# Kernel tuning notes

Hardware: AMD Instinct MI355X
Metric: run time of the kernel (lower is better)

The kernel has to match this reference:

```python
import jax, jax.numpy as jnp
import numpy as np

CLIP_FRAMES = 16
CLIP_STRIDE = 8
D_CODE = 256
K_CODE = 8192
ENC_DIM = 128 * CLIP_FRAMES * 4 * 4  # 32768
EPS = 1e-5


def setup_inputs() -> dict:
    key = jax.random.key(0)
    ks = jax.random.split(key, 16)
    rn = lambda k, s, sc: (jax.random.normal(k, s, jnp.float32) * sc)
    inp = {}
    inp['x'] = jax.random.normal(ks[0], (4, 3, 64, 96, 96), jnp.float32)
    inp['conv1_w'] = rn(ks[1], (32, 3, 3, 3, 3), 0.1)
    inp['conv1_b'] = jnp.zeros((32,), jnp.float32)
    inp['bn1_g'] = jnp.ones((32,), jnp.float32)
    inp['bn1_b'] = jnp.zeros((32,), jnp.float32)
    inp['conv2_w'] = rn(ks[2], (64, 32, 3, 3, 3), 0.05)
    inp['conv2_b'] = jnp.zeros((64,), jnp.float32)
    inp['bn2_g'] = jnp.ones((64,), jnp.float32)
    inp['bn2_b'] = jnp.zeros((64,), jnp.float32)
    inp['conv3_w'] = rn(ks[3], (128, 64, 3, 3, 3), 0.04)
    inp['conv3_b'] = jnp.zeros((128,), jnp.float32)
    inp['bn3_g'] = jnp.ones((128,), jnp.float32)
    inp['bn3_b'] = jnp.zeros((128,), jnp.float32)
    inp['proj_w'] = rn(ks[4], (D_CODE, ENC_DIM), 0.005)
    inp['proj_b'] = jnp.zeros((D_CODE,), jnp.float32)
    inp['codebook'] = jax.random.uniform(ks[5], (K_CODE, D_CODE), jnp.float32, -1.0 / K_CODE, 1.0 / K_CODE)
    inp['gru_w_ih'] = rn(ks[6], (3 * D_CODE, D_CODE), 0.05)
    inp['gru_w_hh'] = rn(ks[7], (3 * D_CODE, D_CODE), 0.05)
    inp['gru_b_ih'] = jnp.zeros((3 * D_CODE,), jnp.float32)
    inp['gru_b_hh'] = jnp.zeros((3 * D_CODE,), jnp.float32)
    return inp


def _conv3d(x, w, b):
    y = jax.lax.conv_general_dilated(x, w, (1, 1, 1), ((1, 1), (1, 1), (1, 1)),
                                     dimension_numbers=('NCDHW', 'OIDHW', 'NCDHW'))
    return y + b[None, :, None, None, None]


def _bn(x, g, b):
    # training-mode BatchNorm3d: batch stats over (N,D,H,W), biased variance
    m = x.mean(axis=(0, 2, 3, 4), keepdims=True)
    v = ((x - m) ** 2).mean(axis=(0, 2, 3, 4), keepdims=True)
    return g[None, :, None, None, None] * (x - m) * jax.lax.rsqrt(v + EPS) + b[None, :, None, None, None]


def _maxpool(x):
    return jax.lax.reduce_window(x, -jnp.inf, jax.lax.max, (1, 1, 1, 2, 2), (1, 1, 1, 2, 2), 'VALID')


def _adaptive_avgpool(x):
    # [N,128,16,24,24] -> [N,128,16,4,4]; 24/4=6 exact window
    s = jax.lax.reduce_window(x, 0.0, jax.lax.add, (1, 1, 1, 6, 6), (1, 1, 1, 6, 6), 'VALID')
    return s / 36.0


def _gru(xs, w_ih, w_hh, b_ih, b_hh):
    # torch GRU, batch_first, h0=0. xs: [B,L,D]
    B, L, D = xs.shape
    gx = jnp.einsum('bld,gd->blg', xs, w_ih) + b_ih  # [B,L,3D]

    def step(h, gx_t):
        gh = h @ w_hh.T + b_hh
        xr, xz, xn = jnp.split(gx_t, 3, axis=-1)
        hr, hz, hn = jnp.split(gh, 3, axis=-1)
        r = jax.nn.sigmoid(xr + hr)
        z = jax.nn.sigmoid(xz + hz)
        n = jnp.tanh(xn + r * hn)
        h2 = (1.0 - z) * n + z * h
        return h2, h2

    h0 = jnp.zeros((B, D), xs.dtype)
    _, ys = jax.lax.scan(step, h0, jnp.swapaxes(gx, 0, 1))
    return jnp.swapaxes(ys, 0, 1)  # [B,L,D]


def _forward(x, conv1_w, conv1_b, bn1_g, bn1_b, conv2_w, conv2_b, bn2_g, bn2_b,
             conv3_w, conv3_b, bn3_g, bn3_b, proj_w, proj_b, codebook,
             gru_w_ih, gru_w_hh, gru_b_ih, gru_b_hh):
    B, C, T, H, W = x.shape
    num_clips = max(1, (T - CLIP_FRAMES) // CLIP_STRIDE + 1)
    clips = jnp.stack([x[:, :, i * CLIP_STRIDE:i * CLIP_STRIDE + CLIP_FRAMES] for i in range(num_clips)])

    def encode(clip):  # clip: [B,3,16,96,96]; BN stats per-clip like the torch loop
        h = jax.nn.relu(_bn(_conv3d(clip, conv1_w, conv1_b), bn1_g, bn1_b))
        h = _maxpool(h)
        h = jax.nn.relu(_bn(_conv3d(h, conv2_w, conv2_b), bn2_g, bn2_b))
        h = _maxpool(h)
        h = jax.nn.relu(_bn(_conv3d(h, conv3_w, conv3_b), bn3_g, bn3_b))
        h = _adaptive_avgpool(h)            # [B,128,16,4,4]
        h = h.reshape(B, -1)                # [B, 32768]
        return h @ proj_w.T + proj_b        # [B, D_CODE]

    features = jnp.swapaxes(jax.vmap(encode)(clips), 0, 1)  # [B,L,D]
    L, D = features.shape[1], features.shape[2]

    # quantize: squared-Euclidean argmin (same argmin as torch.cdist p=2)
    flat = features.reshape(-1, D)
    d2 = (flat * flat).sum(-1, keepdims=True) - 2.0 * flat @ codebook.T + (codebook * codebook).sum(-1)
    token_indices = jnp.argmin(d2, axis=-1)
    quantized = codebook[token_indices].reshape(B, L, D)

    sg = jax.lax.stop_gradient
    commitment_loss = jnp.mean((features - sg(quantized)) ** 2)
    codebook_loss = jnp.mean((quantized - sg(features)) ** 2)
    context_features = _gru(quantized[:, :-1], gru_w_ih, gru_w_hh, gru_b_ih, gru_b_hh)
    context_loss = jnp.mean((context_features - features[:, 1:]) ** 2)
    vq_loss = commitment_loss + 0.25 * codebook_loss + 0.1 * context_loss
    return token_indices.reshape(B, L), quantized, commitment_loss, codebook_loss, context_loss, vq_loss


def reference(x, conv1_w, conv1_b, bn1_g, bn1_b, conv2_w, conv2_b, bn2_g, bn2_b,
              conv3_w, conv3_b, bn3_g, bn3_b, proj_w, proj_b, codebook,
              gru_w_ih, gru_w_hh, gru_b_ih, gru_b_hh):
    return _forward(x, conv1_w, conv1_b, bn1_g, bn1_b, conv2_w, conv2_b, bn2_g, bn2_b,
                    conv3_w, conv3_b, bn3_g, bn3_b, proj_w, proj_b, codebook,
                    gru_w_ih, gru_w_hh, gru_b_ih, gru_b_hh)
```

## Files before the change

### kernel.cpp

```cpp
#include <hip/hip_runtime.h>
#include <math.h>


typedef __attribute__((ext_vector_type(8))) short short8;
typedef __attribute__((ext_vector_type(4))) float f32x4;

__device__ inline unsigned short f2bf(float x) {
    unsigned int u = __float_as_uint(x);
    u += 0x7FFFu + ((u >> 16) & 1u);
    return (unsigned short)(u >> 16);
}
__device__ inline float bf2f(unsigned short h) {
    return __uint_as_float(((unsigned int)h) << 16);
}
__device__ inline f32x4 vmax4(f32x4 a, f32x4 b) {
    return (f32x4){fmaxf(a.x, b.x), fmaxf(a.y, b.y), fmaxf(a.z, b.z), fmaxf(a.w, b.w)};
}
__device__ inline f32x4 vmin4(f32x4 a, f32x4 b) {
    return (f32x4){fminf(a.x, b.x), fminf(a.y, b.y), fminf(a.z, b.z), fminf(a.w, b.w)};
}

#define MF(d, a, b) d = __builtin_amdgcn_mfma_f32_16x16x32_bf16(a, b, d, 0, 0, 0)

#define C1LOADR(J) \
    f32x4 u = *(const f32x4*)(ip + (J) * 36); \
    f32x4 w4 = *(const f32x4*)(ip + (J) * 36 + 4); \
    f32x4 sA = u; \
    f32x4 sB = __builtin_shufflevector(u, w4, 1, 2, 3, 4); \
    f32x4 sC = __builtin_shufflevector(u, w4, 2, 3, 4, 5);
#define C1UPD0(I) a0_##I += wa0 * sA + wa1 * sB + wa2 * sC; a1_##I += wb0 * sA + wb1 * sB + wb2 * sC;
#define C1UPD1(I) a0_##I += wa3 * sA + wa4 * sB + wa5 * sC; a1_##I += wb3 * sA + wb4 * sB + wb5 * sC;
#define C1UPD2(I) a0_##I += wa6 * sA + wa7 * sB + wa8 * sC; a1_##I += wb6 * sA + wb7 * sB + wb8 * sC;

__launch_bounds__(256, 3)
__global__ void conv1k(const float* __restrict__ x, const float* __restrict__ wgt,
                       const float* __restrict__ bias, float* __restrict__ pmax,
                       float* __restrict__ pmin, float* __restrict__ stats, int t0) {
    int bb = blockIdx.x;
    int xt = bb % 3; int yt = (bb / 3) % 4; int t = (bb / 12) % 16; int n = bb / 192;
    int x0 = xt * 32, y0 = yt * 24;
    __shared__ float tile[9 * 936];
    __shared__ float wl[3456];
    __shared__ float sst[64];
    int tid = threadIdx.x;
    for (int i = tid; i < 3456; i += 256) {
        int idx = i % 12; int r = i / 12;
        int co = r & 31; int p = r >> 5;
        wl[i] = idx < 9 ? wgt[co * 81 + p * 9 + idx] : 0.f;
    }
    if (tid < 64) sst[tid] = 0.f;
    for (int i = tid; i < 7956; i += 256) {
        int p = i / 884; int rem = i % 884;
        int r = rem / 34, cl = rem % 34;
        int ci = p / 3, kt = p % 3;
        int lt = t + kt - 1;
        int yy = y0 + r - 1, xx = x0 + cl - 1;
        float v = 0.f;
        if (lt >= 0 && lt <= 15 && yy >= 0 && yy < 96 && xx >= 0 && xx < 96)
            v = x[((size_t)(n * 3 + ci) * 64 + (t0 + lt)) * 9216 + yy * 96 + cl + x0 - 1];
        tile[p * 936 + r * 36 + cl] = v;
    }
    __syncthreads();

    int cg = tid & 15;
    int co0 = cg * 2;
    float bv0 = bias[co0], bv1 = bias[co0 + 1];
    float ls0 = 0.f, lq0 = 0.f, ls1 = 0.f, lq1 = 0.f;
    size_t nt48 = (size_t)(n * 16 + t) * 48;

    #pragma unroll 1
    for (int rr = 0; rr < 3; ++rr) {
        int sp = rr * 16 + (tid >> 4);
        int tx = sp & 7, ty = sp >> 3;
        f32x4 a0_0 = (f32x4)bv0, a0_1 = (f32x4)bv0, a0_2 = (f32x4)bv0, a0_3 = (f32x4)bv0;
        f32x4 a1_0 = (f32x4)bv1, a1_1 = (f32x4)bv1, a1_2 = (f32x4)bv1, a1_3 = (f32x4)bv1;

        #pragma unroll 1
        for (int p = 0; p < 9; ++p) {
            const float* wpk = wl + ((p * 32 + co0) * 12);
            f32x4 wv0 = *(const f32x4*)(wpk);
            f32x4 wv1 = *(const f32x4*)(wpk + 4);
            f32x4 wv2 = *(const f32x4*)(wpk + 8);
            f32x4 wv3 = *(const f32x4*)(wpk + 12);
            f32x4 wv4 = *(const f32x4*)(wpk + 16);
            f32x4 wv5 = *(const f32x4*)(wpk + 20);
            float wa0 = wv0.x, wa1 = wv0.y, wa2 = wv0.z, wa3 = wv0.w;
            float wa4 = wv1.x, wa5 = wv1.y, wa6 = wv1.z, wa7 = wv1.w;
            float wa8 = wv2.x;
            float wb0 = wv3.x, wb1 = wv3.y, wb2 = wv3.z, wb3 = wv3.w;
            float wb4 = wv4.x, wb5 = wv4.y, wb6 = wv4.z, wb7 = wv4.w;
            float wb8 = wv5.x;
            const float* ip = tile + p * 936 + (ty * 4) * 36 + tx * 4;
            { C1LOADR(0) C1UPD0(0) }
            { C1LOADR(1) C1UPD0(1) C1UPD1(0) }
            { C1LOADR(2) C1UPD0(2) C1UPD1(1) C1UPD2(0) }
            { C1LOADR(3) C1UPD0(3) C1UPD1(2) C1UPD2(1) }
            { C1LOADR(4) C1UPD1(3) C1UPD2(2) }
            { C1LOADR(5) C1UPD2(3) }
        }

        f32x4 s4 = a0_0 + a0_1 + a0_2 + a0_3;
        ls0 += s4.x + s4.y + s4.z + s4.w;
        f32x4 q4 = a0_0 * a0_0 + a0_1 * a0_1 + a0_2 * a0_2 + a0_3 * a0_3;
        lq0 += q4.x + q4.y + q4.z + q4.w;
        f32x4 s5 = a1_0 + a1_1 + a1_2 + a1_3;
        ls1 += s5.x + s5.y + s5.z + s5.w;
        f32x4 q5 = a1_0 * a1_0 + a1_1 * a1_1 + a1_2 * a1_2 + a1_3 * a1_3;
        lq1 += q5.x + q5.y + q5.z + q5.w;

        f32x4 mx0a = vmax4(a0_0, a0_1), mx0b = vmax4(a0_2, a0_3);
        f32x4 mn0a = vmin4(a0_0, a0_1), mn0b = vmin4(a0_2, a0_3);
        f32x4 mx1a = vmax4(a1_0, a1_1), mx1b = vmax4(a1_2, a1_3);
        f32x4 mn1a = vmin4(a1_0, a1_1), mn1b = vmin4(a1_2, a1_3);
        size_t row0 = (nt48 + (size_t)(yt * 12 + ty * 2)) * 1536 + (size_t)(xt * 16 + tx * 2) * 32 + co0;
        size_t row1 = row0 + 1536;
        *(float2*)(pmax + row0)      = make_float2(fmaxf(mx0a.x, mx0a.y), fmaxf(mx1a.x, mx1a.y));
        *(float2*)(pmax + row0 + 32) = make_float2(fmaxf(mx0a.z, mx0a.w), fmaxf(mx1a.z, mx1a.w));
        *(float2*)(pmax + row1)      = make_float2(fmaxf(mx0b.x, mx0b.y), fmaxf(mx1b.x, mx1b.y));
        *(float2*)(pmax + row1 + 32) = make_float2(fmaxf(mx0b.z, mx0b.w), fmaxf(mx1b.z, mx1b.w));
        *(float2*)(pmin + row0)      = make_float2(fminf(mn0a.x, mn0a.y), fminf(mn1a.x, mn1a.y));
        *(float2*)(pmin + row0 + 32) = make_float2(fminf(mn0a.z, mn0a.w), fminf(mn1a.z, mn1a.w));
        *(float2*)(pmin + row1)      = make_float2(fminf(mn0b.x, mn0b.y), fminf(mn1b.x, mn1b.y));
        *(float2*)(pmin + row1 + 32) = make_float2(fminf(mn0b.z, mn0b.w), fminf(mn1b.z, mn1b.w));
    }

    ls0 += __shfl_xor(ls0, 16, 64); ls0 += __shfl_xor(ls0, 32, 64);
    lq0 += __shfl_xor(lq0, 16, 64); lq0 += __shfl_xor(lq0, 32, 64);
    ls1 += __shfl_xor(ls1, 16, 64); ls1 += __shfl_xor(ls1, 32, 64);
    lq1 += __shfl_xor(lq1, 16, 64); lq1 += __shfl_xor(lq1, 32, 64);
    if ((tid & 63) < 16) {
        atomicAdd(&sst[co0 * 2], ls0);
        atomicAdd(&sst[co0 * 2 + 1], lq0);
        atomicAdd(&sst[co0 * 2 + 2], ls1);
        atomicAdd(&sst[co0 * 2 + 3], lq1);
    }
    __syncthreads();
    if (tid < 64) atomicAdd(&stats[tid], sst[tid]);
}

__global__ void bnpool1b(const float* __restrict__ pmax, const float* __restrict__ pmin,
                         const float* __restrict__ st, const float* __restrict__ gam,
                         const float* __restrict__ bet,
                         unsigned short* __restrict__ phi, unsigned short* __restrict__ plo) {
    int i = blockIdx.x * 256 + threadIdx.x;
    int c8 = i & 3; int xo = (i >> 2) % 48; int yo = (i / 192) % 48;
    int t = (i / 9216) % 16; int n = i / 147456;
    size_t base = (((size_t)(n * 16 + t) * 48 + yo) * 48 + xo) * 32 + c8 * 8;
    union { unsigned short s[8]; uint4 v; } Uh, Ul;
    #pragma unroll
    for (int j = 0; j < 8; ++j) {
        int ch = c8 * 8 + j;
        float mean = st[ch * 2] * (1.f / 589824.f);
        float var  = st[ch * 2 + 1] * (1.f / 589824.f) - mean * mean;
        var = var < 0.f ? 0.f : var;
        float sc = gam[ch] / sqrtf(var + 1e-5f);
        float sh = bet[ch] - mean * sc;
        float pv = sc >= 0.f ? pmax[base + j] : pmin[base + j];
        float v = fmaxf(sc * pv + sh, 0.f);
        Uh.s[j] = f2bf(v);
        Ul.s[j] = f2bf(v - bf2f(Uh.s[j]));
    }
    size_t off = ((((size_t)n * 18 + t + 1) * 50 + yo + 1) * 52 + (xo + 1)) * 32 + c8 * 8;
    *(uint4*)(phi + off) = Uh.v;
    *(uint4*)(plo + off) = Ul.v;
}

#define DECLW(S) short8 S##a0, S##a1, S##a2, S##a3, S##l0, S##l1, S##l2, S##l3;

#define LOADW2(S, KY, KX) { \
    const unsigned short* wb_ = wkt + ((KY) * 3 + (KX)) * 4096; \
    S##a0 = *(const short8*)(wb_);        S##a1 = *(const short8*)(wb_ + 512); \
    S##a2 = *(const short8*)(wb_ + 1024); S##a3 = *(const short8*)(wb_ + 1536); \
    S##l0 = *(const short8*)(wb_ + 2048); S##l1 = *(const short8*)(wb_ + 2560); \
    S##l2 = *(const short8*)(wb_ + 3072); S##l3 = *(const short8*)(wb_ + 3584); \
}

#define COMPUTE2(S, KY, KX) { \
    int row_ = wv + (KY); \
    int xx0_ = (KX) + c, xx1_ = 16 + (KX) + c, xx2_ = 32 + (KX) + c; \
    int sq0_ = (q ^ (xx0_ & 3) ^ ((xx0_ >> 2) & 3)) << 3; \
    int sq1_ = (q ^ (xx1_ & 3) ^ ((xx1_ >> 2) & 3)) << 3; \
    int sq2_ = (q ^ (xx2_ & 3) ^ ((xx2_ >> 2) & 3)) << 3; \
    short8 bh0_ = *(const short8*)(tin + ((row_ * 52 + xx0_) << 5) + sq0_); \
    short8 bl0_ = *(const short8*)(tin + (((6 + row_) * 52 + xx0_) << 5) + sq0_); \
    short8 bh1_ = *(const short8*)(tin + ((row_ * 52 + xx1_) << 5) + sq1_); \
    short8 bl1_ = *(const short8*)(tin + (((6 + row_) * 52 + xx1_) << 5) + sq1_); \
    short8 bh2_ = *(const short8*)(tin + ((row_ * 52 + xx2_) << 5) + sq2_); \
    short8 bl2_ = *(const short8*)(tin + (((6 + row_) * 52 + xx2_) << 5) + sq2_); \
    MF(acc[0][0], S##a0, bh0_); MF(acc[0][0], S##a0, bl0_); MF(acc[0][0], S##l0, bh0_); \
    MF(acc[0][1], S##a0, bh1_); MF(acc[0][1], S##a0, bl1_); MF(acc[0][1], S##l0, bh1_); \
    MF(acc[0][2], S##a0, bh2_); MF(acc[0][2], S##a0, bl2_); MF(acc[0][2], S##l0, bh2_); \
    MF(acc[1][0], S##a1, bh0_); MF(acc[1][0], S##a1, bl0_); MF(acc[1][0], S##l1, bh0_); \
    MF(acc[1][1], S##a1, bh1_); MF(acc[1][1], S##a1, bl1_); MF(acc[1][1], S##l1, bh1_); \
    MF(acc[1][2], S##a1, bh2_); MF(acc[1][2], S##a1, bl2_); MF(acc[1][2], S##l1, bh2_); \
    MF(acc[2][0], S##a2, bh0_); MF(acc[2][0], S##a2, bl0_); MF(acc[2][0], S##l2, bh0_); \
    MF(acc[2][1], S##a2, bh1_); MF(acc[2][1], S##a2, bl1_); MF(acc[2][1], S##l2, bh1_); \
    MF(acc[2][2], S##a2, bh2_); MF(acc[2][2], S##a2, bl2_); MF(acc[2][2], S##l2, bh2_); \
    MF(acc[3][0], S##a3, bh0_); MF(acc[3][0], S##a3, bl0_); MF(acc[3][0], S##l3, bh0_); \
    MF(acc[3][1], S##a3, bh1_); MF(acc[3][1], S##a3, bl1_); MF(acc[3][1], S##l3, bh1_); \
    MF(acc[3][2], S##a3, bh2_); MF(acc[3][2], S##a3, bl2_); MF(acc[3][2], S##l3, bh2_); \
}

__launch_bounds__(256, 3)
__global__ void conv2k(const unsigned short* __restrict__ phi, const unsigned short* __restrict__ plo,
                       const unsigned short* __restrict__ w2p, const float* __restrict__ bias,
                       float* __restrict__ out, float* __restrict__ st) {
    __shared__ unsigned short tin[2 * 6 * 52 * 32];
    float (*sred)[64] = (float (*)[64])(tin);
    float (*qred)[64] = (float (*)[64])(tin + 512);
    int b = blockIdx.x;
    int k8 = b & 7, i96 = b >> 3;
    int n = k8 >> 1, th = k8 & 1;
    int tt = i96 / 12; int y0 = (i96 - tt * 12) * 4;
    int t = th * 8 + tt;
    int wv = threadIdx.x >> 6, lane = threadIdx.x & 63;
    int c = lane & 15, q = lane >> 4;
    int y = y0 + wv;

    f32x4 acc[4][3];
    #pragma unroll
    for (int i = 0; i < 4; ++i)
        #pragma unroll
        for (int j = 0; j < 3; ++j) acc[i][j] = (f32x4)0.f;

    DECLW(P) DECLW(Q)

    #pragma unroll 1
    for (int kt = 0; kt < 3; ++kt) {
        const unsigned short* srch = phi + (size_t)(n * 18 + t + kt) * (50 * 52 * 32);
        const unsigned short* srcl = plo + (size_t)(n * 18 + t + kt) * (50 * 52 * 32);
        const unsigned short* wkt = w2p + kt * 36864 + c * 32 + q * 8;
        LOADW2(P, 0, 0)
        __syncthreads();
        for (int i = threadIdx.x; i < 2496; i += 256) {
            int g = i & 3; int xx = (i >> 2) % 52; int rh = (i >> 2) / 52;
            int row = rh % 6; int h = rh / 6;
            int sg = g ^ (xx & 3) ^ ((xx >> 2) & 3);
            const unsigned short* src = (h ? srcl : srch) + (size_t)(y0 + row) * 1664 + xx * 32 + g * 8;
            *(uint4*)(tin + ((rh * 52 + xx) << 5) + (sg << 3)) = *(const uint4*)src;
        }
        __syncthreads();
        LOADW2(Q, 0, 1) COMPUTE2(P, 0, 0)
        LOADW2(P, 0, 2) COMPUTE2(Q, 0, 1)
        LOADW2(Q, 1, 0) COMPUTE2(P, 0, 2)
        LOADW2(P, 1, 1) COMPUTE2(Q, 1, 0)
        LOADW2(Q, 1, 2) COMPUTE2(P, 1, 1)
        LOADW2(P, 2, 0) COMPUTE2(Q, 1, 2)
        LOADW2(Q, 2, 1) COMPUTE2(P, 2, 0)
        LOADW2(P, 2, 2) COMPUTE2(Q, 2, 1)
        COMPUTE2(P, 2, 2)
    }
    __syncthreads();
    float* ob = out + (((size_t)(n * 16 + t) * 48) + y) * (48 * 64);
    #pragma unroll
    for (int mb = 0; mb < 4; ++mb) {
        f32x4 bv = *(const f32x4*)(bias + mb * 16 + q * 4);
        f32x4 v0 = acc[mb][0] + bv, v1 = acc[mb][1] + bv, v2 = acc[mb][2] + bv;
        *(f32x4*)(ob + (0 * 16 + c) * 64 + mb * 16 + q * 4) = v0;
        *(f32x4*)(ob + (1 * 16 + c) * 64 + mb * 16 + q * 4) = v1;
        *(f32x4*)(ob + (2 * 16 + c) * 64 + mb * 16 + q * 4) = v2;
        #pragma unroll
        for (int r = 0; r < 4; ++r) {
            float s  = v0[r] + v1[r] + v2[r];
            float q2 = v0[r] * v0[r] + v1[r] * v1[r] + v2[r] * v2[r];
            #pragma unroll
            for (int m = 1; m < 16; m <<= 1) { s += __shfl_xor(s, m, 64); q2 += __shfl_xor(q2, m, 64); }
            if (c == 0) { sred[wv][mb * 16 + q * 4 + r] = s; qred[wv][mb * 16 + q * 4 + r] = q2; }
        }
    }
    __syncthreads();
    if (threadIdx.x < 64) {
        float s = sred[0][threadIdx.x] + sred[1][threadIdx.x] + sred[2][threadIdx.x] + sred[3][threadIdx.x];
        float q2 = qred[0][threadIdx.x] + qred[1][threadIdx.x] + qred[2][threadIdx.x] + qred[3][threadIdx.x];
        atomicAdd(&st[threadIdx.x * 2], s);
        atomicAdd(&st[threadIdx.x * 2 + 1], q2);
    }
}

__global__ void bnpool2k(const float* __restrict__ cin, const float* __restrict__ st,
                         const float* __restrict__ gam, const float* __restrict__ bet,
                         unsigned short* __restrict__ phi, unsigned short* __restrict__ plo) {
    int i = blockIdx.x * 256 + threadIdx.x;
    if (i >= 509184) return;
    int oc = i & 7; int xp = (i >> 3) % 34; int yp = (i / 272) % 26;
    int tp = (i / 7072) % 18; int n = i / 127296;
    union { unsigned short s[8]; uint4 v; } Uh, Ul;
    if (tp >= 1 && tp <= 16 && yp >= 1 && yp <= 24 && xp >= 1 && xp <= 24) {
        int t = tp - 1, yo = yp - 1, xo = xp - 1;
        const float* b0 = cin + ((((size_t)(n * 16 + t) * 48) + 2 * yo) * 48 + 2 * xo) * 64 + oc * 8;
        #pragma unroll
        for (int j = 0; j < 8; ++j) {
            int ch = oc * 8 + j;
            float mean = st[ch * 2] * (1.f / 147456.f);
            float var  = st[ch * 2 + 1] * (1.f / 147456.f) - mean * mean;
            var = var < 0.f ? 0.f : var;
            float sc = gam[ch] / sqrtf(var + 1e-5f);
            float sh = bet[ch] - mean * sc;
            float a  = b0[j] * sc + sh;
            float bb = b0[64 + j] * sc + sh;
            float c2 = b0[3072 + j] * sc + sh;
            float d  = b0[3136 + j] * sc + sh;
            float v = fmaxf(fmaxf(fmaxf(a, bb), fmaxf(c2, d)), 0.f);
            Uh.s[j] = f2bf(v);
            Ul.s[j] = f2bf(v - bf2f(Uh.s[j]));
        }
    } else {
        Uh.v = make_uint4(0, 0, 0, 0);
        Ul.v = make_uint4(0, 0, 0, 0);
    }
    size_t off = ((((size_t)n * 18 + tp) * 26 + yp) * 34 + xp) * 64 + oc * 8;
    *(uint4*)(phi + off) = Uh.v;
    *(uint4*)(plo + off) = Ul.v;
}

#define LOADW3(S, KY, KX, KC) { \
    const unsigned short* wb_ = wkt + (KY) * 24576 + (KX) * 8192 + (KC) * 2048; \
    S##a0 = *(const short8*)(wb_);        S##a1 = *(const short8*)(wb_ + 512); \
    S##a2 = *(const short8*)(wb_ + 1024); S##a3 = *(const short8*)(wb_ + 1536); \
    S##l0 = *(const short8*)(wb_ + 4096); S##l1 = *(const short8*)(wb_ + 4608); \
    S##l2 = *(const short8*)(wb_ + 5120); S##l3 = *(const short8*)(wb_ + 5632); \
}

#define COMPUTE3(S, KY, KX, KC) { \
    int row_ = wv + (KY); \
    int xx0_ = (KX) + c, xx1_ = 16 + (KX) + c; \
    int so0_ = (((KC) * 4 + q) ^ (xx0_ & 7)) << 3; \
    int so1_ = (((KC) * 4 + q) ^ (xx1_ & 7)) << 3; \
    short8 bh0_ = *(const short8*)(tin + ((row_ * 34 + xx0_) << 6) + so0_); \
    short8 bl0_ = *(const short8*)(tin + (((6 + row_) * 34 + xx0_) << 6) + so0_); \
    short8 bh1_ = *(const short8*)(tin + ((row_ * 34 + xx1_) << 6) + so1_); \
    short8 bl1_ = *(const short8*)(tin + (((6 + row_) * 34 + xx1_) << 6) + so1_); \
    MF(acc[0][0], S##a0, bh0_); MF(acc[0][0], S##a0, bl0_); MF(acc[0][0], S##l0, bh0_); \
    MF(acc[0][1], S##a0, bh1_); MF(acc[0][1], S##a0, bl1_); MF(acc[0][1], S##l0, bh1_); \
    MF(acc[1][0], S##a1, bh0_); MF(acc[1][0], S##a1, bl0_); MF(acc[1][0], S##l1, bh0_); \
    MF(acc[1][1], S##a1, bh1_); MF(acc[1][1], S##a1, bl1_); MF(acc[1][1], S##l1, bh1_); \
    MF(acc[2][0], S##a2, bh0_); MF(acc[2][0], S##a2, bl0_); MF(acc[2][0], S##l2, bh0_); \
    MF(acc[2][1], S##a2, bh1_); MF(acc[2][1], S##a2, bl1_); MF(acc[2][1], S##l2, bh1_); \
    MF(acc[3][0], S##a3, bh0_); MF(acc[3][0], S##a3, bl0_); MF(acc[3][0], S##l3, bh0_); \
    MF(acc[3][1], S##a3, bh1_); MF(acc[3][1], S##a3, bl1_); MF(acc[3][1], S##l3, bh1_); \
}

__launch_bounds__(256, 3)
__global__ void conv3k(const unsigned short* __restrict__ phi, const unsigned short* __restrict__ plo,
                       const unsigned short* __restrict__ w3p, const float* __restrict__ bias,
                       float* __restrict__ out, float* __restrict__ st) {
    __shared__ unsigned short tin[2 * 6 * 34 * 64];
    float (*sred)[64] = (float (*)[64])(tin);
    float (*qred)[64] = (float (*)[64])(tin + 512);
    int b = blockIdx.x;
    int k8 = b & 7, i96 = b >> 3;
    int n = k8 >> 1, th = k8 & 1;
    int cg = i96 / 48; int r48 = i96 - cg * 48;
    int tt = r48 / 6;  int y0 = (r48 - tt * 6) * 4;
    int t = th * 8 + tt;
    int wv = threadIdx.x >> 6, lane = threadIdx.x & 63;
    int c = lane & 15, q = lane >> 4;
    int y = y0 + wv;

    f32x4 acc[4][2];
    #pragma unroll
    for (int i = 0; i < 4; ++i) { acc[i][0] = (f32x4)0.f; acc[i][1] = (f32x4)0.f; }

    const unsigned short* wsrc = w3p + (size_t)cg * 221184 + c * 32 + q * 8;
    DECLW(P) DECLW(Q)

    #pragma unroll 1
    for (int kt = 0; kt < 3; ++kt) {
        const unsigned short* srch = phi + (size_t)(n * 18 + t + kt) * (26 * 34 * 64);
        const unsigned short* srcl = plo + (size_t)(n * 18 + t + kt) * (26 * 34 * 64);
        const unsigned short* wkt = wsrc + kt * 73728;
        LOADW3(P, 0, 0, 0)
        __syncthreads();
        for (int i = threadIdx.x; i < 3264; i += 256) {
            int g = i & 7; int xx = (i >> 3) % 34; int rh = (i >> 3) / 34;
            int row = rh % 6; int h = rh / 6;
            const unsigned short* src = (h ? srcl : srch) + (size_t)(y0 + row) * 2176 + xx * 64 + g * 8;
            *(uint4*)(tin + ((rh * 34 + xx) << 6) + ((g ^ (xx & 7)) << 3)) = *(const uint4*)src;
        }
        __syncthreads();
        LOADW3(Q, 0, 0, 1) COMPUTE3(P, 0, 0, 0)
        LOADW3(P, 0, 1, 0) COMPUTE3(Q, 0, 0, 1)
        LOADW3(Q, 0, 1, 1) COMPUTE3(P, 0, 1, 0)
        LOADW3(P, 0, 2, 0) COMPUTE3(Q, 0, 1, 1)
        LOADW3(Q, 0, 2, 1) COMPUTE3(P, 0, 2, 0)
        LOADW3(P, 1, 0, 0) COMPUTE3(Q, 0, 2, 1)
        LOADW3(Q, 1, 0, 1) COMPUTE3(P, 1, 0, 0)
        LOADW3(P, 1, 1, 0) COMPUTE3(Q, 1, 0, 1)
        LOADW3(Q, 1, 1, 1) COMPUTE3(P, 1, 1, 0)
        LOADW3(P, 1, 2, 0) COMPUTE3(Q, 1, 1, 1)
        LOADW3(Q, 1, 2, 1) COMPUTE3(P, 1, 2, 0)
        LOADW3(P, 2, 0, 0) COMPUTE3(Q, 1, 2, 1)
        LOADW3(Q, 2, 0, 1) COMPUTE3(P, 2, 0, 0)
        LOADW3(P, 2, 1, 0) COMPUTE3(Q, 2, 0, 1)
        LOADW3(Q, 2, 1, 1) COMPUTE3(P, 2, 1, 0)
        LOADW3(P, 2, 2, 0) COMPUTE3(Q, 2, 1, 1)
        LOADW3(Q, 2, 2, 1) COMPUTE3(P, 2, 2, 0)
        COMPUTE3(Q, 2, 2, 1)
    }
    __syncthreads();
    float* ob = out + (((size_t)(n * 16 + t) * 24) + y) * (24 * 128) + cg * 64;
    #pragma unroll
    for (int mb = 0; mb < 4; ++mb) {
        f32x4 bv = *(const f32x4*)(bias + cg * 64 + mb * 16 + q * 4);
        f32x4 v0 = acc[mb][0] + bv;
        f32x4 v1 = acc[mb][1] + bv;
        *(f32x4*)(ob + c * 128 + mb * 16 + q * 4) = v0;
        if (c < 8) *(f32x4*)(ob + (16 + c) * 128 + mb * 16 + q * 4) = v1;
        #pragma unroll
        for (int r = 0; r < 4; ++r) {
            float s  = v0[r] + (c < 8 ? v1[r] : 0.f);
            float q2 = v0[r] * v0[r] + (c < 8 ? v1[r] * v1[r] : 0.f);
            #pragma unroll
            for (int m = 1; m < 16; m <<= 1) { s += __shfl_xor(s, m, 64); q2 += __shfl_xor(q2, m, 64); }
            if (c == 0) { sred[wv][mb * 16 + q * 4 + r] = s; qred[wv][mb * 16 + q * 4 + r] = q2; }
        }
    }
    __syncthreads();
    if (threadIdx.x < 64) {
        int co = cg * 64 + threadIdx.x;
        float s = sred[0][threadIdx.x] + sred[1][threadIdx.x] + sred[2][threadIdx.x] + sred[3][threadIdx.x];
        float q2 = qred[0][threadIdx.x] + qred[1][threadIdx.x] + qred[2][threadIdx.x] + qred[3][threadIdx.x];
        atomicAdd(&st[co * 2], s);
        atomicAdd(&st[co * 2 + 1], q2);
    }
}

__global__ void bnavgk(const float* __restrict__ x, const float* __restrict__ st,
                       const float* __restrict__ gam, const float* __restrict__ bet,
                       float* __restrict__ enc) {
    int i = blockIdx.x * 256 + threadIdx.x;
    int c = i & 127; int xo = (i >> 7) & 3; int yo = (i >> 9) & 3;
    int t = (i >> 11) & 15; int n = i >> 15;
    float mean = st[c * 2] * (1.f / 36864.f);
    float var  = st[c * 2 + 1] * (1.f / 36864.f) - mean * mean;
    var = var < 0.f ? 0.f : var;
    float sc = gam[c] / sqrtf(var + 1e-5f);
    float sh = bet[c] - mean * sc;
    const float* base = x + ((((size_t)(n * 16 + t) * 24) + yo * 6) * 24 + xo * 6) * 128 + c;
    float s = 0.f;
    #pragma unroll
    for (int wy = 0; wy < 6; ++wy)
        #pragma unroll
        for (int wx = 0; wx < 6; ++wx)
            s += fmaxf(base[(wy * 24 + wx) * 128] * sc + sh, 0.f);
    enc[(size_t)n * 32768 + (size_t)c * 256 + t * 16 + yo * 4 + xo] = s * (1.f / 36.f);
}

__global__ void prep2k(const float* __restrict__ c2w, unsigned short* __restrict__ w2p) {
    int i = blockIdx.x * 256 + threadIdx.x;
    if (i >= 110592) return;
    int ci = i & 31; int co = (i >> 5) & 63; int h = (i >> 11) & 1;
    int o = (i >> 12) % 9; int kt = i / 36864;
    int ky = o / 3, kx = o % 3;
    float w = c2w[(((size_t)(co * 32 + ci) * 3 + kt) * 3 + ky) * 3 + kx];
    unsigned short hi = f2bf(w);
    w2p[i] = h ? f2bf(w - bf2f(hi)) : hi;
}
__global__ void prep3k(const float* __restrict__ c3w, unsigned short* __restrict__ w3p) {
    int i = blockIdx.x * 256 + threadIdx.x;
    if (i >= 442368) return;
    int cil = i & 31; int cop = (i >> 5) & 63; int kc = (i >> 11) & 1; int h = (i >> 12) & 1;
    int kx = (i >> 13) % 3; int ky = (i / 24576) % 3; int kt = (i / 73728) % 3; int cg = i / 221184;
    int ci = kc * 32 + cil; int co = cg * 64 + cop;
    float w = c3w[(((size_t)(co * 64 + ci) * 3 + kt) * 3 + ky) * 3 + kx];
    unsigned short hi = f2bf(w);
    w3p[i] = h ? f2bf(w - bf2f(hi)) : hi;
}
__global__ void prepwhhk(const float* __restrict__ whh, float* __restrict__ wt) {
    int i = blockIdx.x * 256 + threadIdx.x;
    int g = i % 768, k = i / 768;
    wt[i] = whh[(size_t)g * 256 + k];
}

__global__ void transck(const float* __restrict__ cb, float* __restrict__ cbT) {
    __shared__ float t[32][33];
    int bx = blockIdx.x & 255;
    int by = blockIdx.x >> 8;
    int ld = threadIdx.x & 31, lk = threadIdx.x >> 5;
    #pragma unroll
    for (int i = 0; i < 4; ++i) {
        int kl = lk + i * 8;
        t[kl][ld] = cb[(size_t)(bx * 32 + kl) * 256 + by * 32 + ld];
    }
    __syncthreads();
    #pragma unroll
    for (int i = 0; i < 4; ++i) {
        int dl = lk + i * 8;
        cbT[(size_t)(by * 32 + dl) * 8192 + bx * 32 + ld] = t[ld][dl];
    }
}

__global__ void cnormk(const float* __restrict__ cbT, double* __restrict__ cn2) {
    int k = blockIdx.x * 256 + threadIdx.x;
    double s = 0.0;
    for (int d = 0; d < 256; ++d) {
        double c = (double)cbT[(size_t)d * 8192 + k];
        s += c * c;
    }
    cn2[k] = s;
}

__global__ void projinitk(const float* __restrict__ pb, float* __restrict__ feat) {
    int i = blockIdx.x * 256 + threadIdx.x;
    feat[i] = pb[i & 255];
}

__global__ void projk(const float* __restrict__ enc, const float* __restrict__ pw,
                      float* __restrict__ feat) {
    int d = blockIdx.x & 255; int ch = blockIdx.x >> 8;
    int k0 = ch * 4096;
    float acc[28];
    #pragma unroll
    for (int e = 0; e < 28; ++e) acc[e] = 0.f;
    const float* wrow = pw + (size_t)d * 32768 + k0;
    for (int k = threadIdx.x; k < 4096; k += 256) {
        float wv = wrow[k];
        #pragma unroll
        for (int e = 0; e < 28; ++e) acc[e] += enc[(size_t)e * 32768 + k0 + k] * wv;
    }
    __shared__ float red[4 * 28];
    #pragma unroll
    for (int e = 0; e < 28; ++e) {
        float v = acc[e];
        #pragma unroll
        for (int o = 32; o > 0; o >>= 1) v += __shfl_down(v, o, 64);
        if ((threadIdx.x & 63) == 0) red[(threadIdx.x >> 6) * 28 + e] = v;
    }
    __syncthreads();
    if (threadIdx.x < 28) {
        int e = threadIdx.x;
        int l = e >> 2, n = e & 3;
        float s = red[e] + red[28 + e] + red[56 + e] + red[84 + e];
        atomicAdd(&feat[(size_t)(n * 7 + l) * 256 + d], s);
    }
}

__global__ void quantk(const float* __restrict__ feat, const float* __restrict__ cbT,
                       const double* __restrict__ cn2, unsigned long long* __restrict__ best) {
    int kc = blockIdx.x & 31, r = blockIdx.x >> 5;
    int k = kc * 256 + threadIdx.x;
    __shared__ float fs[256];
    fs[threadIdx.x] = feat[(size_t)r * 256 + threadIdx.x];
    __syncthreads();
    double dot = 0.0;
    for (int d = 0; d < 256; ++d)
        dot += (double)cbT[(size_t)d * 8192 + k] * (double)fs[d];
    float s = (float)(cn2[k] - 2.0 * dot);
    unsigned int bits = __float_as_uint(s);
    unsigned int key = (bits & 0x80000000u) ? ~bits : (bits | 0x80000000u);
    unsigned long long p = ((unsigned long long)key << 32) | (unsigned int)k;
    #pragma unroll
    for (int o = 32; o > 0; o >>= 1) {
        unsigned long long qv = __shfl_down(p, o, 64);
        if (qv < p) p = qv;
    }
    if ((threadIdx.x & 63) == 0) atomicMin(&best[r], p);
}

__global__ void gatherk(const unsigned long long* __restrict__ best,
                        const float* __restrict__ feat, const float* __restrict__ cb,
                        float* __restrict__ dout, float* __restrict__ quant,
                        float* __restrict__ acc) {
    int r = blockIdx.x;
    int d = threadIdx.x;
    int idx = (int)(best[r] & 0xFFFFFFFFull);
    float q = cb[(size_t)idx * 256 + d];
    quant[r * 256 + d] = q;
    dout[28 + r * 256 + d] = q;
    if (d == 0) dout[r] = (float)idx;
    float df = feat[r * 256 + d] - q;
    float v = df * df;
    #pragma unroll
    for (int o = 32; o > 0; o >>= 1) v += __shfl_down(v, o, 64);
    if ((d & 63) == 0) atomicAdd(&acc[0], v);
}

__global__ void gxk(const float* __restrict__ quant, const float* __restrict__ wih,
                    const float* __restrict__ bih, float* __restrict__ gx) {
    int o = blockIdx.x * 256 + threadIdx.x;
    int g = o % 768; int t = (o / 768) % 6; int n = o / (768 * 6);
    const float* q = quant + (size_t)(n * 7 + t) * 256;
    const float* w = wih + (size_t)g * 256;
    float s = bih[g];
    #pragma unroll 4
    for (int d = 0; d < 256; ++d) s += q[d] * w[d];
    gx[o] = s;
}

__global__ void gru_allk(const float* __restrict__ gx, const float* __restrict__ wt,
                         const float* __restrict__ bhh, const float* __restrict__ feat,
                         float* __restrict__ acc) {
    int b = blockIdx.x;
    int d = threadIdx.x;
    __shared__ float hs[256];
    hs[d] = 0.f;
    __syncthreads();
    float ctx = 0.f;
    for (int t = 0; t < 6; ++t) {
        float g0 = bhh[d], g1 = bhh[256 + d], g2 = bhh[512 + d];
        #pragma unroll 4
        for (int k = 0; k < 256; ++k) {
            float hv = hs[k];
            const float* wr = wt + (size_t)k * 768;
            g0 += wr[d] * hv; g1 += wr[256 + d] * hv; g2 += wr[512 + d] * hv;
        }
        const float* gxr = gx + (size_t)(b * 6 + t) * 768;
        float xr = gxr[d], xz = gxr[256 + d], xn = gxr[512 + d];
        float rr = 1.f / (1.f + expf(-(xr + g0)));
        float zz = 1.f / (1.f + expf(-(xz + g1)));
        float nn = tanhf(xn + rr * g2);
        float h2 = (1.f - zz) * nn + zz * hs[d];
        __syncthreads();
        hs[d] = h2;
        __syncthreads();
        float df = h2 - feat[(size_t)(b * 7 + t + 1) * 256 + d];
        ctx += df * df;
    }
    #pragma unroll
    for (int o = 32; o > 0; o >>= 1) ctx += __shfl_down(ctx, o, 64);
    if ((d & 63) == 0) atomicAdd(&acc[1], ctx);
}

__global__ void fink(const float* __restrict__ acc, float* __restrict__ dout) {
    float comm = acc[0] / 7168.f;
    float ctx  = acc[1] / 6144.f;
    dout[7196] = comm;
    dout[7197] = comm;
    dout[7198] = ctx;
    dout[7199] = comm + 0.25f * comm + 0.1f * ctx;
}

extern "C" void kernel_launch(void* const* d_in, const int* in_sizes, int n_in,
                              void* d_out, int out_size, void* d_ws, size_t ws_size,
                              hipStream_t stream) {
    (void)in_sizes; (void)n_in; (void)out_size; (void)ws_size;
    const float* x    = (const float*)d_in[0];
    const float* c1w  = (const float*)d_in[1];
    const float* c1b  = (const float*)d_in[2];
    const float* bn1g = (const float*)d_in[3];
    const float* bn1b = (const float*)d_in[4];
    const float* c2w  = (const float*)d_in[5];
    const float* c2b  = (const float*)d_in[6];
    const float* bn2g = (const float*)d_in[7];
    const float* bn2b = (const float*)d_in[8];
    const float* c3w  = (const float*)d_in[9];
    const float* c3b  = (const float*)d_in[10];
    const float* bn3g = (const float*)d_in[11];
    const float* bn3b = (const float*)d_in[12];
    const float* pw   = (const float*)d_in[13];
    const float* pb   = (const float*)d_in[14];
    const float* cb   = (const float*)d_in[15];
    const float* wih  = (const float*)d_in[16];
    const float* whh  = (const float*)d_in[17];
    const float* bih  = (const float*)d_in[18];
    const float* bhh  = (const float*)d_in[19];
    float* out = (float*)d_out;

    char* w = (char*)d_ws;
    float* A  = (float*)w;                         w += 75497472;
    float* PMAX = A;
    float* PMIN = A + 4718592;
    float* cbT = A;
    double* cn2 = (double*)((char*)A + 8388608);
    char*  SH = w;                                 w += 16293888;
    unsigned short* P3h = (unsigned short*)SH;
    unsigned short* P3l = (unsigned short*)(SH + 8146944);
    unsigned short* P2h = (unsigned short*)w;      w += 11980800;
    unsigned short* P2l = (unsigned short*)w;      w += 11980800;
    unsigned short* W2P = (unsigned short*)w;      w += 221184;
    unsigned short* W3P = (unsigned short*)w;      w += 884736;
    float* WT    = (float*)w;                      w += 786432;
    float* enc   = (float*)w;                      w += 3670016;
    float* feat  = (float*)w;                      w += 28672;
    float* quant = (float*)w;                      w += 28672;
    float* gx    = (float*)w;                      w += 73728;
    float* statsA = (float*)w;                     w += 21504;
    float* acc    = (float*)w;                     w += 16;
    unsigned long long* best = (unsigned long long*)w;  w += 224;

    hipMemsetAsync(P2h, 0, 11980800 * 2, stream);
    hipMemsetAsync(statsA, 0, 21504 + 16, stream);
    hipMemsetAsync(best, 0xFF, 224, stream);
    prep2k<<<432, 256, 0, stream>>>(c2w, W2P);
    prep3k<<<1728, 256, 0, stream>>>(c3w, W3P);
    prepwhhk<<<768, 256, 0, stream>>>(whh, WT);

    for (int l = 0; l < 7; ++l) {
        float* st1 = statsA + (l * 3 + 0) * 256;
        float* st2 = statsA + (l * 3 + 1) * 256;
        float* st3 = statsA + (l * 3 + 2) * 256;
        conv1k<<<768, 256, 0, stream>>>(x, c1w, c1b, PMAX, PMIN, st1, l * 8);
        bnpool1b<<<2304, 256, 0, stream>>>(PMAX, PMIN, st1, bn1g, bn1b, P2h, P2l);
        conv2k<<<768, 256, 0, stream>>>(P2h, P2l, W2P, c2b, A, st2);
        bnpool2k<<<1989, 256, 0, stream>>>(A, st2, bn2g, bn2b, P3h, P3l);
        conv3k<<<768, 256, 0, stream>>>(P3h, P3l, W3P, c3b, A, st3);
        bnavgk<<<512, 256, 0, stream>>>(A, st3, bn3g, bn3b, enc + (size_t)l * 131072);
    }

    transck<<<2048, 256, 0, stream>>>(cb, cbT);
    cnormk<<<32, 256, 0, stream>>>(cbT, cn2);
    projinitk<<<28, 256, 0, stream>>>(pb, feat);
    projk<<<2048, 256, 0, stream>>>(enc, pw, feat);
    quantk<<<896, 256, 0, stream>>>(feat, cbT, cn2, best);
    gatherk<<<28, 256, 0, stream>>>(best, feat, cb, out, quant, acc);
    gxk<<<72, 256, 0, stream>>>(quant, wih, bih, gx);
    gru_allk<<<4, 256, 0, stream>>>(gx, WT, bhh, feat, acc);
    fink<<<1, 1, 0, stream>>>(acc, out);
}
```

Measured before the change: 2.305 ms.

## Shrink conv3 LDS tile and drop manual weight double-buffering for higher occupancy

The conv3 kernel now stages only the 26 x-columns it actually reads (instead of 34), shrinking the shared-memory tile. The hand-unrolled ping-pong weight prefetch macros are replaced by a plain ky/kx/kc loop that loads the weights just before use, which cuts register pressure. Launch bounds rise from 3 to 4 blocks per SIMD/CU. Together these aim for more resident waves to hide latency, at the cost of losing the explicit software pipelining of weight loads and adding a clamp on the x index.

Result: no change. 2.316 ms (+0.5%).

```diff
diff --git a/kernel.cpp b/kernel.cpp
--- a/kernel.cpp
+++ b/kernel.cpp
@@ -313,38 +313,11 @@
     *(uint4*)(plo + off) = Ul.v;
 }
 
-#define LOADW3(S, KY, KX, KC) { \
-    const unsigned short* wb_ = wkt + (KY) * 24576 + (KX) * 8192 + (KC) * 2048; \
-    S##a0 = *(const short8*)(wb_);        S##a1 = *(const short8*)(wb_ + 512); \
-    S##a2 = *(const short8*)(wb_ + 1024); S##a3 = *(const short8*)(wb_ + 1536); \
-    S##l0 = *(const short8*)(wb_ + 4096); S##l1 = *(const short8*)(wb_ + 4608); \
-    S##l2 = *(const short8*)(wb_ + 5120); S##l3 = *(const short8*)(wb_ + 5632); \
-}
-
-#define COMPUTE3(S, KY, KX, KC) { \
-    int row_ = wv + (KY); \
-    int xx0_ = (KX) + c, xx1_ = 16 + (KX) + c; \
-    int so0_ = (((KC) * 4 + q) ^ (xx0_ & 7)) << 3; \
-    int so1_ = (((KC) * 4 + q) ^ (xx1_ & 7)) << 3; \
-    short8 bh0_ = *(const short8*)(tin + ((row_ * 34 + xx0_) << 6) + so0_); \
-    short8 bl0_ = *(const short8*)(tin + (((6 + row_) * 34 + xx0_) << 6) + so0_); \
-    short8 bh1_ = *(const short8*)(tin + ((row_ * 34 + xx1_) << 6) + so1_); \
-    short8 bl1_ = *(const short8*)(tin + (((6 + row_) * 34 + xx1_) << 6) + so1_); \
-    MF(acc[0][0], S##a0, bh0_); MF(acc[0][0], S##a0, bl0_); MF(acc[0][0], S##l0, bh0_); \
-    MF(acc[0][1], S##a0, bh1_); MF(acc[0][1], S##a0, bl1_); MF(acc[0][1], S##l0, bh1_); \
-    MF(acc[1][0], S##a1, bh0_); MF(acc[1][0], S##a1, bl0_); MF(acc[1][0], S##l1, bh0_); \
-    MF(acc[1][1], S##a1, bh1_); MF(acc[1][1], S##a1, bl1_); MF(acc[1][1], S##l1, bh1_); \
-    MF(acc[2][0], S##a2, bh0_); MF(acc[2][0], S##a2, bl0_); MF(acc[2][0], S##l2, bh0_); \
-    MF(acc[2][1], S##a2, bh1_); MF(acc[2][1], S##a2, bl1_); MF(acc[2][1], S##l2, bh1_); \
-    MF(acc[3][0], S##a3, bh0_); MF(acc[3][0], S##a3, bl0_); MF(acc[3][0], S##l3, bh0_); \
-    MF(acc[3][1], S##a3, bh1_); MF(acc[3][1], S##a3, bl1_); MF(acc[3][1], S##l3, bh1_); \
-}
-
-__launch_bounds__(256, 3)
+__launch_bounds__(256, 4)
 __global__ void conv3k(const unsigned short* __restrict__ phi, const unsigned short* __restrict__ plo,
                        const unsigned short* __restrict__ w3p, const float* __restrict__ bias,
                        float* __restrict__ out, float* __restrict__ st) {
-    __shared__ unsigned short tin[2 * 6 * 34 * 64];
+    __shared__ unsigned short tin[12 * 26 * 64];
     float (*sred)[64] = (float (*)[64])(tin);
     float (*qred)[64] = (float (*)[64])(tin + 512);
     int b = blockIdx.x;
@@ -362,40 +335,54 @@
     for (int i = 0; i < 4; ++i) { acc[i][0] = (f32x4)0.f; acc[i][1] = (f32x4)0.f; }
 
     const unsigned short* wsrc = w3p + (size_t)cg * 221184 + c * 32 + q * 8;
-    DECLW(P) DECLW(Q)
 
     #pragma unroll 1
     for (int kt = 0; kt < 3; ++kt) {
         const unsigned short* srch = phi + (size_t)(n * 18 + t + kt) * (26 * 34 * 64);
         const unsigned short* srcl = plo + (size_t)(n * 18 + t + kt) * (26 * 34 * 64);
         const unsigned short* wkt = wsrc + kt * 73728;
-        LOADW3(P, 0, 0, 0)
         __syncthreads();
-        for (int i = threadIdx.x; i < 3264; i += 256) {
-            int g = i & 7; int xx = (i >> 3) % 34; int rh = (i >> 3) / 34;
+        for (int i = threadIdx.x; i < 2496; i += 256) {
+            int g = i & 7; int xx = (i >> 3) % 26; int rh = (i >> 3) / 26;
             int row = rh % 6; int h = rh / 6;
             const unsigned short* src = (h ? srcl : srch) + (size_t)(y0 + row) * 2176 + xx * 64 + g * 8;
-            *(uint4*)(tin + ((rh * 34 + xx) << 6) + ((g ^ (xx & 7)) << 3)) = *(const uint4*)src;
+            *(uint4*)(tin + ((rh * 26 + xx) << 6) + ((g ^ (xx & 7)) << 3)) = *(const uint4*)src;
         }
         __syncthreads();
-        LOADW3(Q, 0, 0, 1) COMPUTE3(P, 0, 0, 0)
-        LOADW3(P, 0, 1, 0) COMPUTE3(Q, 0, 0, 1)
-        LOADW3(Q, 0, 1, 1) COMPUTE3(P, 0, 1, 0)
-        LOADW3(P, 0, 2, 0) COMPUTE3(Q, 0, 1, 1)
-        LOADW3(Q, 0, 2, 1) COMPUTE3(P, 0, 2, 0)
-        LOADW3(P, 1, 0, 0) COMPUTE3(Q, 0, 2, 1)
-        LOADW3(Q, 1, 0, 1) COMPUTE3(P, 1, 0, 0)
-        LOADW3(P, 1, 1, 0) COMPUTE3(Q, 1, 0, 1)
-        LOADW3(Q, 1, 1, 1) COMPUTE3(P, 1, 1, 0)
-        LOADW3(P, 1, 2, 0) COMPUTE3(Q, 1, 1, 1)
-        LOADW3(Q, 1, 2, 1) COMPUTE3(P, 1, 2, 0)
-        LOADW3(P, 2, 0, 0) COMPUTE3(Q, 1, 2, 1)
-        LOADW3(Q, 2, 0, 1) COMPUTE3(P, 2, 0, 0)
-        LOADW3(P, 2, 1, 0) COMPUTE3(Q, 2, 0, 1)
-        LOADW3(Q, 2, 1, 1) COMPUTE3(P, 2, 1, 0)
-        LOADW3(P, 2, 2, 0) COMPUTE3(Q, 2, 1, 1)
-        LOADW3(Q, 2, 2, 1) COMPUTE3(P, 2, 2, 0)
-        COMPUTE3(Q, 2, 2, 1)
+        #pragma unroll 1
+        for (int ky = 0; ky < 3; ++ky) {
+            int row = wv + ky;
+            const unsigned short* wky = wkt + ky * 24576;
+            #pragma unroll
+            for (int kx = 0; kx < 3; ++kx) {
+                #pragma unroll
+                for (int kc = 0; kc < 2; ++kc) {
+                    const unsigned short* wb = wky + kx * 8192 + kc * 2048;
+                    short8 ah[4], al[4], bh[2], bl[2];
+                    #pragma unroll
+                    for (int mb = 0; mb < 4; ++mb) {
+                        ah[mb] = *(const short8*)(wb + mb * 512);
+                        al[mb] = *(const short8*)(wb + 4096 + mb * 512);
+                    }
+                    #pragma unroll
+                    for (int xt = 0; xt < 2; ++xt) {
+                        int xr = xt * 16 + kx + c;
+                        int xx = xr > 25 ? 25 : xr;
+                        int so = ((kc * 4 + q) ^ (xx & 7)) << 3;
+                        bh[xt] = *(const short8*)(tin + ((row * 26 + xx) << 6) + so);
+                        bl[xt] = *(const short8*)(tin + (((6 + row) * 26 + xx) << 6) + so);
+                    }
+                    #pragma unroll
+                    for (int mb = 0; mb < 4; ++mb)
+                        #pragma unroll
+                        for (int xt = 0; xt < 2; ++xt) {
+                            MF(acc[mb][xt], ah[mb], bh[xt]);
+                            MF(acc[mb][xt], ah[mb], bl[xt]);
+                            MF(acc[mb][xt], al[mb], bh[xt]);
+                        }
+                }
+            }
+        }
     }
     __syncthreads();
     float* ob = out + (((size_t)(n * 16 + t) * 24) + y) * (24 * 128) + cg * 64;
```
